# Optimization experiments

Measured on AMD Instinct MI355X. Metric: run time of the kernel, lower is better.

## Reference

```python
import jax, jax.numpy as jnp
import numpy as np

G = 8      # conv groups
NG = 32    # groupnorm groups
H = 8      # attention heads
EPS = 1e-5
SLOPE = 0.1

def _qkv_branch(x, w, b, gw, gb):
    # x: [B, Cin, P]; w: [Cout, Cin//G]; grouped 1x1 conv == block matmul
    B, Cin, P = x.shape
    Cout = w.shape[0]
    xg = x.reshape(B, G, Cin // G, P)
    wg = w.reshape(G, Cout // G, Cin // G)
    y = jnp.einsum('gof,bgfp->bgop', wg, xg).reshape(B, Cout, P) + b[None, :, None]
    # GroupNorm(NG, Cout)
    yg = y.reshape(B, NG, Cout // NG, P)
    mu = yg.mean(axis=(2, 3), keepdims=True)
    var = yg.var(axis=(2, 3), keepdims=True)
    yn = ((yg - mu) * jax.lax.rsqrt(var + EPS)).reshape(B, Cout, P)
    yn = yn * gw[None, :, None] + gb[None, :, None]
    # LeakyReLU(0.1)
    return jnp.where(yn >= 0, yn, SLOPE * yn)

def setup_inputs() -> dict:
    key = jax.random.key(0)
    ks = jax.random.split(key, 14)
    B, Cin, Cout, P = 8, 512, 1024, 2048
    x = jax.random.normal(ks[0], (B, Cin, P), dtype=jnp.float32)
    def conv_w(k):
        return jax.random.normal(k, (Cout, Cin // G), dtype=jnp.float32) * 0.02
    inp = {
        'x': x,
        'wq': conv_w(ks[1]), 'bq': jnp.zeros((Cout,), jnp.float32),
        'gw1': jnp.ones((Cout,), jnp.float32), 'gb1': jnp.zeros((Cout,), jnp.float32),
        'wk': conv_w(ks[2]), 'bk': jnp.zeros((Cout,), jnp.float32),
        'gw2': jnp.ones((Cout,), jnp.float32), 'gb2': jnp.zeros((Cout,), jnp.float32),
        'wv': conv_w(ks[3]), 'bv': jnp.zeros((Cout,), jnp.float32),
        'gw3': jnp.ones((Cout,), jnp.float32), 'gb3': jnp.zeros((Cout,), jnp.float32),
    }
    return inp

def reference(x, wq, bq, gw1, gb1, wk, bk, gw2, gb2, wv, bv, gw3, gb3):
    Q = _qkv_branch(x, wq, bq, gw1, gb1)   # [B, C, P]
    K = _qkv_branch(x, wk, bk, gw2, gb2)
    V = _qkv_branch(x, wv, bv, gw3, gb3)
    B, C, P = K.shape
    d = C // H
    Qh = Q.reshape(B, H, d, P)
    Kh = K.reshape(B, H, d, P)
    Vh = V.reshape(B, H, d, P)
    scale = 1.0 / np.sqrt(C / H).astype(np.float32)
    scores = jnp.einsum('bhci,bhcj->bhij', Kh, Vh) * scale  # [B,H,P,P]
    A = jax.nn.softmax(scores, axis=-1)
    out = jnp.einsum('bhij,bhcj->bhci', A, Qh)              # [B,H,d,P]
    return out.reshape(B, C, P)
```

## Files before the change

kernel.cpp:

```cpp
#include <hip/hip_runtime.h>

typedef unsigned short ushort_t;
typedef float  f32x4   __attribute__((ext_vector_type(4)));
typedef float  f32x16  __attribute__((ext_vector_type(16)));
typedef __bf16 bf16x4  __attribute__((ext_vector_type(4)));
typedef __bf16 bf16x8  __attribute__((ext_vector_type(8)));
typedef unsigned uint2v __attribute__((ext_vector_type(2)));

#define MFMA16(a,b,c) __builtin_amdgcn_mfma_f32_16x16x32_bf16((a),(b),(c),0,0,0)
#define MFMA32(a,b,c) __builtin_amdgcn_mfma_f32_32x32x16_bf16((a),(b),(c),0,0,0)

__device__ __forceinline__ ushort_t f2bf(float f) {
  union { float f; unsigned u; } v; v.f = f;
  unsigned u = v.u;
  unsigned r = u + 0x7FFFu + ((u >> 16) & 1u);
  return (ushort_t)(r >> 16);
}
__device__ __forceinline__ float bf2f(ushort_t s) {
  union { unsigned u; float f; } v; v.u = ((unsigned)s) << 16;
  return v.f;
}

__device__ __forceinline__ void plswap(unsigned& a, unsigned& b) {
#if __has_builtin(__builtin_amdgcn_permlane32_swap)
  uint2v r = __builtin_amdgcn_permlane32_swap(a, b, false, false);
  a = r[0]; b = r[1];
#else
  asm("v_permlane32_swap_b32 %0, %1" : "+v"(a), "+v"(b));
#endif
}

__device__ __forceinline__ void gload_lds16(const ushort_t* g, ushort_t* l) {
  __builtin_amdgcn_global_load_lds(
      (const __attribute__((address_space(1))) unsigned int*)g,
      (__attribute__((address_space(3))) unsigned int*)l, 16, 0, 0);
}

__global__ __launch_bounds__(256) void conv_gn(
    const float* __restrict__ x,
    const float* __restrict__ wq, const float* __restrict__ wk, const float* __restrict__ wv,
    const float* __restrict__ bq, const float* __restrict__ bk, const float* __restrict__ bv,
    ushort_t* __restrict__ Qb, ushort_t* __restrict__ Kb, ushort_t* __restrict__ Vb,
    float* __restrict__ stats) {
  int pc = blockIdx.x;
  int gz = blockIdx.y;
  int b = gz & 7, g = gz >> 3;
  int tid = threadIdx.x, lane = tid & 63, wid = tid >> 6;
  int l15 = lane & 15, q = lane >> 4;

  __shared__ __align__(16) ushort_t xl[128 * 72];
  __shared__ __align__(16) ushort_t wl[128 * 72];
  __shared__ __align__(16) ushort_t yl[128 * 40];
  __shared__ float biasl[128];
  __shared__ float redbuf[8];

  const float* xsrc = x + ((size_t)(b * 512 + g * 64)) * 2048 + pc * 128;
#pragma unroll
  for (int r = 0; r < 8; ++r) {
    int chunk = tid + 256 * r;
    int c = chunk >> 5, p4 = chunk & 31;
    float4 v = *(const float4*)&xsrc[(size_t)c * 2048 + p4 * 4];
    xl[(p4 * 4 + 0) * 72 + c] = f2bf(v.x);
    xl[(p4 * 4 + 1) * 72 + c] = f2bf(v.y);
    xl[(p4 * 4 + 2) * 72 + c] = f2bf(v.z);
    xl[(p4 * 4 + 3) * 72 + c] = f2bf(v.w);
  }
  __syncthreads();

  bf16x8 Bx[2][2];
#pragma unroll
  for (int n2 = 0; n2 < 2; ++n2)
#pragma unroll
    for (int kk = 0; kk < 2; ++kk)
      Bx[n2][kk] = *(const bf16x8*)&xl[((wid * 2 + n2) * 16 + l15) * 72 + kk * 32 + q * 8];

  for (int br = 0; br < 3; ++br) {
    const float* w    = (br == 0) ? wq : ((br == 1) ? wk : wv);
    const float* bias = (br == 0) ? bq : ((br == 1) ? bk : bv);
    ushort_t* dst     = (br == 0) ? Qb : ((br == 1) ? Kb : Vb);
    __syncthreads();
    const float* wsrc = w + (size_t)g * 128 * 64;
#pragma unroll
    for (int r = 0; r < 8; ++r) {
      int idx = (tid + 256 * r) << 2;
      float4 v = *(const float4*)&wsrc[idx];
      int row = idx >> 6, f = idx & 63;
      bf16x4 wv4 = {(__bf16)v.x, (__bf16)v.y, (__bf16)v.z, (__bf16)v.w};
      *(bf16x4*)&wl[row * 72 + f] = wv4;
    }
    if (tid < 128) biasl[tid] = bias[g * 128 + tid];
    __syncthreads();

    for (int ngs = 0; ngs < 4; ++ngs) {
      int co0 = ngs * 32;
      bf16x8 Aw[2][2];
#pragma unroll
      for (int m = 0; m < 2; ++m)
#pragma unroll
        for (int kk = 0; kk < 2; ++kk)
          Aw[m][kk] = *(const bf16x8*)&wl[(co0 + m * 16 + l15) * 72 + kk * 32 + q * 8];
      f32x4 acc[2][2];
#pragma unroll
      for (int a = 0; a < 2; ++a)
#pragma unroll
        for (int c2 = 0; c2 < 2; ++c2) acc[a][c2] = (f32x4){0.f, 0.f, 0.f, 0.f};
      if (br == 0) {
#pragma unroll
        for (int kk = 0; kk < 2; ++kk)
#pragma unroll
          for (int n2 = 0; n2 < 2; ++n2)
#pragma unroll
            for (int mw = 0; mw < 2; ++mw)
              acc[n2][mw] = MFMA16(Bx[n2][kk], Aw[mw][kk], acc[n2][mw]);
      } else {
#pragma unroll
        for (int kk = 0; kk < 2; ++kk)
#pragma unroll
          for (int n2 = 0; n2 < 2; ++n2)
#pragma unroll
            for (int m = 0; m < 2; ++m)
              acc[m][n2] = MFMA16(Aw[m][kk], Bx[n2][kk], acc[m][n2]);
      }

      float s1 = 0.f, s2 = 0.f;
      if (br == 0) {
#pragma unroll
        for (int n2 = 0; n2 < 2; ++n2)
#pragma unroll
          for (int mw = 0; mw < 2; ++mw) {
            float bi = biasl[co0 + mw * 16 + l15];
#pragma unroll
            for (int rg = 0; rg < 4; ++rg) {
              float y = acc[n2][mw][rg] + bi;
              acc[n2][mw][rg] = y;
              s1 += y; s2 += y * y;
            }
          }
      } else {
#pragma unroll
        for (int m = 0; m < 2; ++m)
#pragma unroll
          for (int n2 = 0; n2 < 2; ++n2)
#pragma unroll
            for (int rg = 0; rg < 4; ++rg) {
              float y = acc[m][n2][rg] + biasl[co0 + m * 16 + 4 * q + rg];
              acc[m][n2][rg] = y;
              s1 += y; s2 += y * y;
            }
      }
#pragma unroll
      for (int mask = 32; mask >= 1; mask >>= 1) {
        s1 += __shfl_xor(s1, mask, 64);
        s2 += __shfl_xor(s2, mask, 64);
      }

      __syncthreads();
      if (lane == 0) { redbuf[wid * 2] = s1; redbuf[wid * 2 + 1] = s2; }
      if (br == 0) {
#pragma unroll
        for (int n2 = 0; n2 < 2; ++n2)
#pragma unroll
          for (int mw = 0; mw < 2; ++mw) {
            bf16x4 pk = {(__bf16)acc[n2][mw][0], (__bf16)acc[n2][mw][1],
                         (__bf16)acc[n2][mw][2], (__bf16)acc[n2][mw][3]};
            *(bf16x4*)&yl[(mw * 16 + l15) * 136 + (wid * 2 + n2) * 16 + 4 * q] = pk;
          }
      } else {
#pragma unroll
        for (int m = 0; m < 2; ++m)
#pragma unroll
          for (int n2 = 0; n2 < 2; ++n2) {
            bf16x4 pk = {(__bf16)acc[m][n2][0], (__bf16)acc[m][n2][1],
                         (__bf16)acc[m][n2][2], (__bf16)acc[m][n2][3]};
            *(bf16x4*)&yl[((wid * 2 + n2) * 16 + l15) * 40 + m * 16 + 4 * q] = pk;
          }
      }
      __syncthreads();

      if (br == 0) {
#pragma unroll
        for (int r = 0; r < 2; ++r) {
          int chunk = tid + 256 * r;
          int row = chunk >> 4, ch = chunk & 15;
          *(uint4*)&dst[((size_t)(b * 1024 + g * 128 + co0 + row)) * 2048 + pc * 128 + ch * 8] =
              *(const uint4*)&yl[row * 136 + ch * 8];
        }
      } else {
#pragma unroll
        for (int r = 0; r < 2; ++r) {
          int chunk = tid + 256 * r;
          int row = chunk >> 2, ch = chunk & 3;
          *(uint4*)&dst[((size_t)(b * 8 + g) * 2048 + pc * 128 + row) * 128 + co0 + ch * 8] =
              *(const uint4*)&yl[row * 40 + ch * 8];
        }
      }
      if (tid == 0) {
        float S1 = redbuf[0] + redbuf[2] + redbuf[4] + redbuf[6];
        float S2 = redbuf[1] + redbuf[3] + redbuf[5] + redbuf[7];
        int sidx = (br * 8 + b) * 32 + g * 4 + ngs;
        atomicAdd(&stats[2 * sidx], S1);
        atomicAdd(&stats[2 * sidx + 1], S2);
      }
    }
  }
}

__global__ __launch_bounds__(256) void gn_apply(
    ushort_t* __restrict__ buf, const float* __restrict__ stats,
    const float* __restrict__ gw1, const float* __restrict__ gb1,
    const float* __restrict__ gw2, const float* __restrict__ gb2,
    const float* __restrict__ gw3, const float* __restrict__ gb3) {
  const unsigned NQ = 16777216u;
  unsigned base = blockIdx.x * 256 + threadIdx.x;
  for (int itn = 0; itn < 12; ++itn) {
    unsigned gid = base + (unsigned)itn * 524288u;
    unsigned e = gid * 8;
    int br; unsigned local;
    if (e < NQ)            { br = 0; local = e; }
    else if (e < 2u * NQ)  { br = 1; local = e - NQ; }
    else                   { br = 2; local = e - 2u * NQ; }
    int b, c0;
    if (br == 0) { b = local >> 21; c0 = (local >> 11) & 1023; }
    else {
      int cih = local & 127; int h = (local >> 18) & 7;
      b = local >> 21; c0 = h * 128 + cih;
    }
    int ng = c0 >> 5;
    const float* gw = (br == 0) ? gw1 : ((br == 1) ? gw2 : gw3);
    const float* gb = (br == 0) ? gb1 : ((br == 1) ? gb2 : gb3);
    int sidx = (br * 8 + b) * 32 + ng;
    float mean = stats[2 * sidx] * (1.f / 65536.f);
    float var  = stats[2 * sidx + 1] * (1.f / 65536.f) - mean * mean;
    float rstd = rsqrtf(var + 1e-5f);
    uint4 d = *(uint4*)&buf[(size_t)e];
    ushort_t* pu = (ushort_t*)&d;
#pragma unroll
    for (int i = 0; i < 8; ++i) {
      int ci = (br == 0) ? c0 : (c0 + i);
      float a = rstd * gw[ci];
      float b2 = gb[ci] - mean * a;
      float yn = fmaf(bf2f(pu[i]), a, b2);
      yn = (yn >= 0.f) ? yn : 0.1f * yn;
      pu[i] = f2bf(yn);
    }
    *(uint4*)&buf[(size_t)e] = d;
  }
}

__global__ __launch_bounds__(256, 2) void attn(
    const ushort_t* __restrict__ Qb, const ushort_t* __restrict__ Kb,
    const ushort_t* __restrict__ Vb, float* __restrict__ out) {
  __shared__ __align__(16) ushort_t fKs[2][32 * 128];
  __shared__ __align__(16) ushort_t Vs[2][128 * 32];

  int lin = blockIdx.x + 8 * blockIdx.y;
  int it = (lin >> 3) & 7;
  int bh = (lin & 7) + 8 * (lin >> 6);
  int b = bh >> 3, h = bh & 7;
  int tid = threadIdx.x, lane = tid & 63, wid = tid >> 6;
  int l31 = lane & 31, q2 = lane >> 5;
  const float sl = 0.08838834764831845f * 1.4426950408889634f;

  bf16x8 Bq[2][8];
#pragma unroll
  for (int nt = 0; nt < 2; ++nt) {
    const ushort_t* fQp =
        Kb + ((size_t)bh * 2048 + it * 256 + wid * 64 + nt * 32 + l31) * 128 + q2 * 8;
#pragma unroll
    for (int dc = 0; dc < 8; ++dc) Bq[nt][dc] = *(const bf16x8*)&fQp[dc * 16];
  }

  float m2[2], l_i[2];
  m2[0] = m2[1] = -3e38f;
  l_i[0] = l_i[1] = 0.f;
  f32x16 O[4][2];
#pragma unroll
  for (int mt = 0; mt < 4; ++mt)
#pragma unroll
    for (int nt = 0; nt < 2; ++nt) O[mt][nt] = (f32x16)(0.f);

  const ushort_t* fKg = Vb + (size_t)bh * 2048 * 128;
  const ushort_t* fVg = Qb + ((size_t)(b * 1024 + h * 128)) * 2048;

#define STAGE(JT, NB)                                                          \
  do {                                                                         \
    _Pragma("unroll")                                                          \
    for (int r = 0; r < 2; ++r) {                                              \
      int n = tid + 256 * r;                                                   \
      int kr = n >> 4, ku = (n & 15) ^ (kr & 7);                               \
      gload_lds16(fKg + (size_t)(JT) * 4096 + kr * 128 + ku * 8,               \
                  &fKs[NB][n * 8]);                                            \
      int vr = n >> 2, vu = (n & 3) ^ ((vr >> 1) & 3);                         \
      gload_lds16(fVg + (size_t)vr * 2048 + (JT) * 32 + vu * 8,                \
                  &Vs[NB][n * 8]);                                             \
    }                                                                          \
  } while (0)

  STAGE(0, 0);
  __syncthreads();
  int cur = 0;

  for (int jt = 0; jt < 64; ++jt) {
    if (jt < 63) STAGE(jt + 1, cur ^ 1);

    f32x16 ST[2];
    ST[0] = (f32x16)(0.f);
    ST[1] = (f32x16)(0.f);
    __builtin_amdgcn_s_setprio(1);
#pragma unroll
    for (int dc = 0; dc < 8; ++dc) {
      int up = (dc * 2 + q2) ^ (l31 & 7);
      bf16x8 Ak = *(const bf16x8*)&fKs[cur][l31 * 128 + up * 8];
      ST[0] = MFMA32(Ak, Bq[0][dc], ST[0]);
      ST[1] = MFMA32(Ak, Bq[1][dc], ST[1]);
    }
    __builtin_amdgcn_s_setprio(0);

    bf16x8 Bp[2][2];
#pragma unroll
    for (int nt = 0; nt < 2; ++nt) {
      float vmax = ST[nt][0];
#pragma unroll
      for (int rg = 1; rg < 16; ++rg) vmax = fmaxf(vmax, ST[nt][rg]);
      float v2 = vmax * sl;
      v2 = fmaxf(v2, __shfl_xor(v2, 32, 64));
      float al = 1.f;
      bool need = !__all(v2 <= m2[nt] + 8.f);
      if (need) {
        float mn2 = fmaxf(m2[nt], v2);
        al = __builtin_amdgcn_exp2f(m2[nt] - mn2);
        m2[nt] = mn2;
      }
      float mn = m2[nt];
      float p16[16];
      float rs = 0.f;
#pragma unroll
      for (int rg = 0; rg < 16; ++rg) {
        p16[rg] = __builtin_amdgcn_exp2f(fmaf(ST[nt][rg], sl, -mn));
        rs += p16[rg];
      }
      rs += __shfl_xor(rs, 32, 64);
      l_i[nt] = l_i[nt] * al + rs;
      if (need) {
#pragma unroll
        for (int mt = 0; mt < 4; ++mt)
#pragma unroll
          for (int rg = 0; rg < 16; ++rg) O[mt][nt][rg] *= al;
      }
#pragma unroll
      for (int jc = 0; jc < 2; ++jc) {
        unsigned pa, pb, pc_, pd;
        asm("v_cvt_pk_bf16_f32 %0, %1, %2"
            : "=v"(pa) : "v"(p16[jc * 8 + 0]), "v"(p16[jc * 8 + 1]));
        asm("v_cvt_pk_bf16_f32 %0, %1, %2"
            : "=v"(pc_) : "v"(p16[jc * 8 + 2]), "v"(p16[jc * 8 + 3]));
        asm("v_cvt_pk_bf16_f32 %0, %1, %2"
            : "=v"(pb) : "v"(p16[jc * 8 + 4]), "v"(p16[jc * 8 + 5]));
        asm("v_cvt_pk_bf16_f32 %0, %1, %2"
            : "=v"(pd) : "v"(p16[jc * 8 + 6]), "v"(p16[jc * 8 + 7]));
        plswap(pa, pb);
        plswap(pc_, pd);
        union { unsigned u[4]; bf16x8 v; } fr;
        fr.u[0] = pa; fr.u[1] = pc_; fr.u[2] = pb; fr.u[3] = pd;
        Bp[nt][jc] = fr.v;
      }
    }

    __builtin_amdgcn_s_setprio(1);
#pragma unroll
    for (int jc = 0; jc < 2; ++jc) {
#pragma unroll
      for (int mt = 0; mt < 4; ++mt) {
        int row = mt * 32 + l31;
        int up = (jc * 2 + q2) ^ ((row >> 1) & 3);
        bf16x8 Av = *(const bf16x8*)&Vs[cur][row * 32 + up * 8];
        O[mt][0] = MFMA32(Av, Bp[0][jc], O[mt][0]);
        O[mt][1] = MFMA32(Av, Bp[1][jc], O[mt][1]);
      }
    }
    __builtin_amdgcn_s_setprio(0);
    __syncthreads();
    cur ^= 1;
  }
#undef STAGE

  float linv[2];
  linv[0] = 1.f / l_i[0];
  linv[1] = 1.f / l_i[1];
#pragma unroll
  for (int mt = 0; mt < 4; ++mt)
#pragma unroll
    for (int nt = 0; nt < 2; ++nt) {
      float* obase = out + ((size_t)(b * 1024 + h * 128 + mt * 32)) * 2048 +
                     it * 256 + wid * 64 + nt * 32 + l31;
#pragma unroll
      for (int rg = 0; rg < 16; ++rg) {
        int c = (rg & 3) + 8 * (rg >> 2) + 4 * q2;
        obase[(size_t)c * 2048] = O[mt][nt][rg] * linv[nt];
      }
    }
}

extern "C" void kernel_launch(void* const* d_in, const int* in_sizes, int n_in,
                              void* d_out, int out_size, void* d_ws, size_t ws_size,
                              hipStream_t stream) {
  const float* x   = (const float*)d_in[0];
  const float* wq  = (const float*)d_in[1];
  const float* bq  = (const float*)d_in[2];
  const float* gw1 = (const float*)d_in[3];
  const float* gb1 = (const float*)d_in[4];
  const float* wk  = (const float*)d_in[5];
  const float* bk  = (const float*)d_in[6];
  const float* gw2 = (const float*)d_in[7];
  const float* gb2 = (const float*)d_in[8];
  const float* wv  = (const float*)d_in[9];
  const float* bv  = (const float*)d_in[10];
  const float* gw3 = (const float*)d_in[11];
  const float* gb3 = (const float*)d_in[12];
  float* out = (float*)d_out;
  char* ws = (char*)d_ws;

  ushort_t* Qb = (ushort_t*)(ws);
  ushort_t* Kb = (ushort_t*)(ws + 33554432);
  ushort_t* Vb = (ushort_t*)(ws + 67108864);
  float* stats = (float*)(ws + 100663296);

  hipMemsetAsync(stats, 0, 1536 * sizeof(float), stream);
  conv_gn<<<dim3(16, 64), 256, 0, stream>>>(x, wq, wk, wv, bq, bk, bv,
                                            Qb, Kb, Vb, stats);
  gn_apply<<<2048, 256, 0, stream>>>(Qb, stats, gw1, gb1, gw2, gb2, gw3, gb3);
  attn<<<dim3(8, 64), 256, 0, stream>>>(Qb, Kb, Vb, out);
}
```

Before: 409.5 us.

## Fuse K-branch GroupNorm into attention Q-fragment load and alias conv staging buffer

The GroupNorm+LeakyReLU pass for the K branch (the one attention loads into registers once per block) moves out of gn_apply and into the attn kernel, which applies it to the register-resident fragments after loading them. gn_apply now touches only the Q and V buffers, cutting one third of its read-modify-write traffic. In conv_gn, the output staging buffer now aliases the input tile's shared memory and the barriers are rearranged, lowering LDS use. The cost is redundant per-block normalization math in attn, plus a hazard that xl is overwritten while later branches still need it. That is safe only because the B fragments are held in registers.

```diff
diff --git a/kernel.cpp b/kernel.cpp
--- a/kernel.cpp
+++ b/kernel.cpp
@@ -50,9 +50,9 @@
 
   __shared__ __align__(16) ushort_t xl[128 * 72];
   __shared__ __align__(16) ushort_t wl[128 * 72];
-  __shared__ __align__(16) ushort_t yl[128 * 40];
   __shared__ float biasl[128];
   __shared__ float redbuf[8];
+  ushort_t* yl = xl;
 
   const float* xsrc = x + ((size_t)(b * 512 + g * 64)) * 2048 + pc * 128;
 #pragma unroll
@@ -78,7 +78,6 @@
     const float* w    = (br == 0) ? wq : ((br == 1) ? wk : wv);
     const float* bias = (br == 0) ? bq : ((br == 1) ? bk : bv);
     ushort_t* dst     = (br == 0) ? Qb : ((br == 1) ? Kb : Vb);
-    __syncthreads();
     const float* wsrc = w + (size_t)g * 128 * 64;
 #pragma unroll
     for (int r = 0; r < 8; ++r) {
@@ -153,9 +152,8 @@
         s1 += __shfl_xor(s1, mask, 64);
         s2 += __shfl_xor(s2, mask, 64);
       }
-
-      __syncthreads();
       if (lane == 0) { redbuf[wid * 2] = s1; redbuf[wid * 2 + 1] = s2; }
+
       if (br == 0) {
 #pragma unroll
         for (int n2 = 0; n2 < 2; ++n2)
@@ -201,6 +199,7 @@
         atomicAdd(&stats[2 * sidx], S1);
         atomicAdd(&stats[2 * sidx + 1], S2);
       }
+      __syncthreads();
     }
   }
 }
@@ -208,17 +207,15 @@
 __global__ __launch_bounds__(256) void gn_apply(
     ushort_t* __restrict__ buf, const float* __restrict__ stats,
     const float* __restrict__ gw1, const float* __restrict__ gb1,
-    const float* __restrict__ gw2, const float* __restrict__ gb2,
     const float* __restrict__ gw3, const float* __restrict__ gb3) {
   const unsigned NQ = 16777216u;
   unsigned base = blockIdx.x * 256 + threadIdx.x;
-  for (int itn = 0; itn < 12; ++itn) {
+  for (int itn = 0; itn < 8; ++itn) {
     unsigned gid = base + (unsigned)itn * 524288u;
-    unsigned e = gid * 8;
-    int br; unsigned local;
-    if (e < NQ)            { br = 0; local = e; }
-    else if (e < 2u * NQ)  { br = 1; local = e - NQ; }
-    else                   { br = 2; local = e - 2u * NQ; }
+    unsigned e2 = gid * 8;
+    int br; unsigned local; size_t addr;
+    if (e2 < NQ) { br = 0; local = e2;      addr = e2; }
+    else         { br = 2; local = e2 - NQ; addr = (size_t)e2 + NQ; }
     int b, c0;
     if (br == 0) { b = local >> 21; c0 = (local >> 11) & 1023; }
     else {
@@ -226,13 +223,13 @@
       b = local >> 21; c0 = h * 128 + cih;
     }
     int ng = c0 >> 5;
-    const float* gw = (br == 0) ? gw1 : ((br == 1) ? gw2 : gw3);
-    const float* gb = (br == 0) ? gb1 : ((br == 1) ? gb2 : gb3);
+    const float* gw = (br == 0) ? gw1 : gw3;
+    const float* gb = (br == 0) ? gb1 : gb3;
     int sidx = (br * 8 + b) * 32 + ng;
     float mean = stats[2 * sidx] * (1.f / 65536.f);
     float var  = stats[2 * sidx + 1] * (1.f / 65536.f) - mean * mean;
     float rstd = rsqrtf(var + 1e-5f);
-    uint4 d = *(uint4*)&buf[(size_t)e];
+    uint4 d = *(uint4*)&buf[addr];
     ushort_t* pu = (ushort_t*)&d;
 #pragma unroll
     for (int i = 0; i < 8; ++i) {
@@ -243,13 +240,15 @@
       yn = (yn >= 0.f) ? yn : 0.1f * yn;
       pu[i] = f2bf(yn);
     }
-    *(uint4*)&buf[(size_t)e] = d;
+    *(uint4*)&buf[addr] = d;
   }
 }
 
 __global__ __launch_bounds__(256, 2) void attn(
     const ushort_t* __restrict__ Qb, const ushort_t* __restrict__ Kb,
-    const ushort_t* __restrict__ Vb, float* __restrict__ out) {
+    const ushort_t* __restrict__ Vb, const float* __restrict__ stats,
+    const float* __restrict__ gw2, const float* __restrict__ gb2,
+    float* __restrict__ out) {
   __shared__ __align__(16) ushort_t fKs[2][32 * 128];
   __shared__ __align__(16) ushort_t Vs[2][128 * 32];
 
@@ -268,6 +267,34 @@
         Kb + ((size_t)bh * 2048 + it * 256 + wid * 64 + nt * 32 + l31) * 128 + q2 * 8;
 #pragma unroll
     for (int dc = 0; dc < 8; ++dc) Bq[nt][dc] = *(const bf16x8*)&fQp[dc * 16];
+  }
+  {
+    float mean4[4], rstd4[4];
+#pragma unroll
+    for (int gi = 0; gi < 4; ++gi) {
+      int sidx = (1 * 8 + b) * 32 + h * 4 + gi;
+      float mean = stats[2 * sidx] * (1.f / 65536.f);
+      float var  = stats[2 * sidx + 1] * (1.f / 65536.f) - mean * mean;
+      mean4[gi] = mean;
+      rstd4[gi] = rsqrtf(var + 1e-5f);
+    }
+#pragma unroll
+    for (int dc = 0; dc < 8; ++dc) {
+      int d0 = dc * 16 + q2 * 8;
+      int gi = d0 >> 5;
+#pragma unroll
+      for (int e = 0; e < 8; ++e) {
+        int c0 = h * 128 + d0 + e;
+        float a  = rstd4[gi] * gw2[c0];
+        float b2 = gb2[c0] - mean4[gi] * a;
+        float v0 = fmaf((float)Bq[0][dc][e], a, b2);
+        float v1 = fmaf((float)Bq[1][dc][e], a, b2);
+        v0 = fmaxf(v0, 0.1f * v0);
+        v1 = fmaxf(v1, 0.1f * v1);
+        Bq[0][dc][e] = (__bf16)v0;
+        Bq[1][dc][e] = (__bf16)v1;
+      }
+    }
   }
 
   float m2[2], l_i[2];
@@ -428,6 +455,6 @@
   hipMemsetAsync(stats, 0, 1536 * sizeof(float), stream);
   conv_gn<<<dim3(16, 64), 256, 0, stream>>>(x, wq, wk, wv, bq, bk, bv,
                                             Qb, Kb, Vb, stats);
-  gn_apply<<<2048, 256, 0, stream>>>(Qb, stats, gw1, gb1, gw2, gb2, gw3, gb3);
-  attn<<<dim3(8, 64), 256, 0, stream>>>(Qb, Kb, Vb, out);
-}
+  gn_apply<<<2048, 256, 0, stream>>>(Qb, stats, gw1, gb1, gw3, gb3);
+  attn<<<dim3(8, 64), 256, 0, stream>>>(Qb, Kb, Vb, stats, gw2, gb2, out);
+}
```

Result: faster. 372.2 us (-9.1%).
